# Performance work log

Measured on AMD Instinct MI355X. Metric: run time of the kernel, lower is better.

## Reference

```python
import jax, jax.numpy as jnp
import numpy as np

NUM_HEADS = 16


def rotate_half(x):
    # '... (j d) -> ... j d' with j=2: split last dim into two halves
    x1, x2 = jnp.split(x, 2, axis=-1)
    return jnp.concatenate([-x2, x1], axis=-1)


def apply_rotary_pos_emb(pos, t):
    # pos: [L, d] broadcast onto t: [B, H, L, d]
    return t * jnp.cos(pos) + rotate_half(t) * jnp.sin(pos)


def setup_inputs() -> dict:
    key = jax.random.key(0)
    ks = jax.random.split(key, 10)
    B, N, KV_N, C = 2, 2048, 2048, 1024
    hd = C // NUM_HEADS
    q = jax.random.normal(ks[0], (B, N, C), dtype=jnp.float32)
    k = jax.random.normal(ks[1], (B, KV_N, C), dtype=jnp.float32)
    v = jax.random.normal(ks[2], (B, KV_N, C), dtype=jnp.float32)
    mask = jax.random.randint(ks[3], (B, KV_N), 0, 2) > 0
    pos_emb = jax.random.normal(ks[4], (KV_N, hd), dtype=jnp.float32)
    s = 1.0 / np.sqrt(C)
    qW = jax.random.normal(ks[5], (C, C), dtype=jnp.float32) * s
    kW = jax.random.normal(ks[6], (C, C), dtype=jnp.float32) * s
    vW = jax.random.normal(ks[7], (C, C), dtype=jnp.float32) * s
    projW = jax.random.normal(ks[8], (C, C), dtype=jnp.float32) * s
    return {"q": q, "k": k, "v": v, "mask": mask, "pos_emb": pos_emb,
            "qW": qW, "kW": kW, "vW": vW, "projW": projW}


def reference(q, k, v, mask, pos_emb, qW, kW, vW, projW):
    B, N, C = q.shape
    H = NUM_HEADS
    hd = C // H
    scale = hd ** -0.5
    # linear projections (no bias)
    q = q @ qW
    k = k @ kW
    v = v @ vW
    # b l (h d) -> b h l d
    split = lambda t: t.reshape(t.shape[0], t.shape[1], H, hd).transpose(0, 2, 1, 3)
    q, k, v = split(q), split(k), split(v)
    q = q * scale
    # inline RoPE on q and k
    q = apply_rotary_pos_emb(pos_emb[:q.shape[-2]], q)
    k = apply_rotary_pos_emb(pos_emb[:k.shape[-2]], k)
    attn = jnp.einsum('bhid,bhjd->bhij', q, k)
    mask_value = -jnp.finfo(attn.dtype).max
    attn = jnp.where(mask[:, None, None, :], attn, mask_value)
    attn = jax.nn.softmax(attn, axis=-1)
    x = jnp.einsum('bhij,bhjd->bhid', attn, v)
    x = x.transpose(0, 2, 1, 3).reshape(B, N, C)
    return x @ projW
```

## Files before the change

kernel.cpp:

```cpp
#include <hip/hip_runtime.h>
#include <hip/hip_bf16.h>

#define BB 2
#define NN 2048
#define KVN 2048
#define CC 1024
#define HH 16
#define HD 64

typedef __bf16 bf16;
typedef __attribute__((ext_vector_type(4))) __bf16 bf16x4;
typedef __attribute__((ext_vector_type(8))) __bf16 bf16x8;
typedef __attribute__((ext_vector_type(4))) float f32x4;

__device__ __forceinline__ void gload_lds16(const void* g, void* l) {
  __builtin_amdgcn_global_load_lds(
      (const __attribute__((address_space(1))) void*)g,
      (__attribute__((address_space(3))) void*)l, 16, 0, 0);
}

__global__ __launch_bounds__(256)
void wtrans(const float* __restrict__ qW, const float* __restrict__ kW,
            const float* __restrict__ vW, const float* __restrict__ pW,
            bf16* __restrict__ Wt) {
  __shared__ bf16 t[64][72];
  const float* in = (blockIdx.z == 0) ? qW : (blockIdx.z == 1) ? kW
                    : (blockIdx.z == 2) ? vW : pW;
  bf16* out = Wt + (size_t)blockIdx.z * CC * CC;
  int r0 = blockIdx.y * 64, c0 = blockIdx.x * 64;
  int tid = threadIdx.x;
  int lr = tid >> 3, lc = (tid & 7) * 8;
  for (int p = 0; p < 2; ++p) {
    int rr = lr + p * 32;
    const float* src = &in[(size_t)(r0 + rr) * CC + c0 + lc];
    float4 a = *(const float4*)src;
    float4 b = *(const float4*)(src + 4);
    t[lc + 0][rr] = (bf16)a.x; t[lc + 1][rr] = (bf16)a.y;
    t[lc + 2][rr] = (bf16)a.z; t[lc + 3][rr] = (bf16)a.w;
    t[lc + 4][rr] = (bf16)b.x; t[lc + 5][rr] = (bf16)b.y;
    t[lc + 6][rr] = (bf16)b.z; t[lc + 7][rr] = (bf16)b.w;
  }
  __syncthreads();
  for (int p = 0; p < 2; ++p) {
    int rr = lr + p * 32;
    *(bf16x8*)&out[(size_t)(c0 + rr) * CC + r0 + lc] = *(const bf16x8*)&t[rr][lc];
  }
}

__global__ __launch_bounds__(256, 3)
void gemm_qkv(const float* __restrict__ qin, const float* __restrict__ kin,
              const float* __restrict__ vin, const bf16* __restrict__ Wt,
              const float* __restrict__ pos, bf16* __restrict__ Qp,
              bf16* __restrict__ Kp, bf16* __restrict__ Vp) {
  __shared__ bf16 As[128 * 64];
  __shared__ bf16 Bs[128 * 64];
  const int bid = blockIdx.x;
  const int u = bid & 7, s = bid >> 3;
  const int nblk = s >> 2;
  const int m0 = (u * 4 + (s & 3)) * 128;
  const int z = nblk >> 3;
  const int n0 = (nblk & 7) * 128;
  const float* A = (z == 0) ? qin : (z == 1) ? kin : vin;
  const bf16* Bt = Wt + (size_t)z * CC * CC;
  bf16* Out = (z == 0) ? Qp : (z == 1) ? Kp : Vp;
  const int tid = threadIdx.x;
  const int wave = tid >> 6, lane = tid & 63;
  const int quad = lane >> 4, l15 = lane & 15;
  const int waveM = (wave >> 1) * 64, waveN = (wave & 1) * 64;
  f32x4 acc[4][4] = {};

  for (int k0 = 0; k0 < CC; k0 += 64) {
#pragma unroll
    for (int p = 0; p < 4; ++p) {
      int ch = p * 256 + tid;
      int r = ch >> 3, c = (ch & 7) ^ (r & 7);
      gload_lds16(Bt + (size_t)(n0 + r) * CC + k0 + c * 8, &Bs[ch * 8]);
    }
#pragma unroll
    for (int p = 0; p < 4; ++p) {
      int ch = p * 256 + tid;
      int r = ch >> 3, c = (ch & 7) ^ (r & 7);
      const float* src = A + (size_t)(m0 + r) * CC + k0 + c * 8;
      float4 a0 = *(const float4*)src;
      float4 a1 = *(const float4*)(src + 4);
      bf16x8 t;
      t[0] = (bf16)a0.x; t[1] = (bf16)a0.y; t[2] = (bf16)a0.z; t[3] = (bf16)a0.w;
      t[4] = (bf16)a1.x; t[5] = (bf16)a1.y; t[6] = (bf16)a1.z; t[7] = (bf16)a1.w;
      *(bf16x8*)&As[ch * 8] = t;
    }
    __syncthreads();
    bf16x8 af[4][2], bfr[4][2];
#pragma unroll
    for (int i = 0; i < 4; ++i) {
      int rA = waveM + i * 16 + l15;
      af[i][0] = *(const bf16x8*)&As[(rA * 8 + (quad ^ (rA & 7))) * 8];
      af[i][1] = *(const bf16x8*)&As[(rA * 8 + ((quad + 4) ^ (rA & 7))) * 8];
      int rB = waveN + i * 16 + l15;
      bfr[i][0] = *(const bf16x8*)&Bs[(rB * 8 + (quad ^ (rB & 7))) * 8];
      bfr[i][1] = *(const bf16x8*)&Bs[(rB * 8 + ((quad + 4) ^ (rB & 7))) * 8];
    }
#pragma unroll
    for (int mi = 0; mi < 4; ++mi)
#pragma unroll
      for (int ni = 0; ni < 4; ++ni) {
        acc[mi][ni] = __builtin_amdgcn_mfma_f32_16x16x32_bf16(
            af[mi][0], bfr[ni][0], acc[mi][ni], 0, 0, 0);
        acc[mi][ni] = __builtin_amdgcn_mfma_f32_16x16x32_bf16(
            af[mi][1], bfr[ni][1], acc[mi][ni], 0, 0, 0);
      }
    __syncthreads();
  }
  const float scale = (z == 0) ? 0.125f : 1.0f;
#pragma unroll
  for (int mi = 0; mi < 4; ++mi) {
#pragma unroll
    for (int r = 0; r < 4; ++r) {
      int m = m0 + waveM + mi * 16 + quad * 4 + r;
      int l = m & (NN - 1);
      if (z == 2) {
#pragma unroll
        for (int ni = 0; ni < 4; ++ni)
          Out[(size_t)m * CC + n0 + waveN + ni * 16 + l15] = (bf16)acc[mi][ni][r];
      } else {
#pragma unroll
        for (int ni = 0; ni < 2; ++ni) {
          int col = n0 + waveN + ni * 16 + l15;
          int d = ni * 16 + l15;
          float x1 = acc[mi][ni][r], x2 = acc[mi][ni + 2][r];
          float s1, c1, s2f, c2f;
          __sincosf(pos[l * HD + d], &s1, &c1);
          __sincosf(pos[l * HD + d + 32], &s2f, &c2f);
          Out[(size_t)m * CC + col]      = (bf16)((x1 * c1 - x2 * s1) * scale);
          Out[(size_t)m * CC + col + 32] = (bf16)((x2 * c2f + x1 * s2f) * scale);
        }
      }
    }
  }
}

__global__ __launch_bounds__(256)
void kpack_kernel(const bf16* __restrict__ Kp, bf16* __restrict__ Kpack) {
  int tix = blockIdx.x, h = blockIdx.y, b = blockIdx.z;
  int bh = b * HH + h;
#pragma unroll
  for (int p = 0; p < 2; ++p) {
    int sp = p * 256 + threadIdx.x;
    int fs = sp >> 6, lane = sp & 63, quad = (sp >> 4) & 3, l15 = sp & 15;
    int ni = fs >> 1, hf = fs & 1;
    bf16x8 v = *(const bf16x8*)&Kp[((size_t)(b * KVN + tix * 64 + ni * 16 + l15)) * CC
                                   + h * HD + hf * 32 + quad * 8];
    *(bf16x8*)&Kpack[(((size_t)(bh * 32 + tix)) * 8 + fs) * 512 + lane * 8] = v;
  }
}

__global__ __launch_bounds__(256)
void vpack_kernel(const bf16* __restrict__ Vp, const int* __restrict__ mask,
                  bf16* __restrict__ VpA, bf16* __restrict__ VpB) {
  __shared__ bf16 t[64][80];
  int tix = blockIdx.x, h = blockIdx.y, b = blockIdx.z;
  int j0 = tix * 64, bh = b * HH + h;
  const int* maskb = mask + b * KVN;
  int tid = threadIdx.x;
  int lr = tid >> 3, lc = (tid & 7) * 8;
  for (int p = 0; p < 2; ++p) {
    int j = lr + p * 32;
    int mv = maskb[j0 + j];
    bf16x8 v = *(const bf16x8*)&Vp[(size_t)(b * KVN + j0 + j) * CC + h * HD + lc];
#pragma unroll
    for (int uu = 0; uu < 8; ++uu) t[lc + uu][j] = mv ? v[uu] : (bf16)0.f;
  }
  __syncthreads();
  for (int p = 0; p < 3; ++p) {
    int sp = p * 256 + tid;
    if (sp < 640) {
      int fs = sp >> 6, lane = sp & 63, quad = (sp >> 4) & 3, l15 = sp & 15;
      int ni = fs >> 1, hf = fs & 1;
      bf16x8 v;
      if (ni < 4) {
        v = *(const bf16x8*)&t[ni * 16 + l15][hf * 32 + quad * 8];
      } else {
#pragma unroll
        for (int jj = 0; jj < 8; ++jj)
          v[jj] = (l15 == 0) ? (bf16)(float)maskb[j0 + hf * 32 + quad * 8 + jj]
                             : (bf16)0.f;
      }
      bf16* dst = (fs < 6) ? (VpA + (size_t)fs * (1 << 19))
                           : (VpB + (size_t)(fs - 6) * (1 << 19));
      *(bf16x8*)&dst[((size_t)(bh * 32 + tix)) * 512 + lane * 8] = v;
    }
  }
}

__global__ __launch_bounds__(256, 2)
void attn3(const bf16* __restrict__ Qp, const bf16* __restrict__ Kpack,
           const bf16* __restrict__ VpA, const bf16* __restrict__ VpB,
           bf16* __restrict__ X) {
  __shared__ char smem[49152];
  const int tid = threadIdx.x, wave = tid >> 6, lane = tid & 63;
  const int quad = lane >> 4, l15 = lane & 15;
  const int bid = blockIdx.x;
  const int u = bid & 7, s = bid >> 3;
  const int bh = u * 4 + (s & 3), qp = s >> 2;
  const int b = bh >> 4, h = bh & 15;
  const int qc = qp * 2 + (wave >> 1), kh = wave & 1;
  const int q0 = qc * 64;
  const int sw = 2 * (l15 & 7);

  bf16* P = (bf16*)(smem + wave * 2048);
  float* mrg = (float*)(smem + 8192);

  bf16x8 qa[4][2];
#pragma unroll
  for (int g = 0; g < 4; ++g) {
    const bf16* qrow = Qp + ((size_t)(b * NN) + q0 + g * 16 + l15) * CC + h * HD;
    qa[g][0] = *(const bf16x8*)&qrow[quad * 8];
    qa[g][1] = *(const bf16x8*)&qrow[32 + quad * 8];
  }

  f32x4 Oacc[4][5] = {};
  const bf16* kbase = Kpack + (size_t)bh * 32 * 8 * 512;

  for (int it = 0; it < 16; ++it) {
    int t = kh * 16 + it;
    bf16x8 kb[8], vb[10];
#pragma unroll
    for (int fs = 0; fs < 8; ++fs)
      kb[fs] = *(const bf16x8*)&kbase[((size_t)t * 8 + fs) * 512 + lane * 8];
#pragma unroll
    for (int fs = 0; fs < 10; ++fs) {
      const bf16* vbs = (fs < 6) ? (VpA + (size_t)fs * (1 << 19))
                                 : (VpB + (size_t)(fs - 6) * (1 << 19));
      vb[fs] = *(const bf16x8*)&vbs[((size_t)(bh * 32 + t)) * 512 + lane * 8];
    }
#pragma unroll
    for (int g = 0; g < 4; ++g) {
      f32x4 sg[4];
#pragma unroll
      for (int ni = 0; ni < 4; ++ni) {
        f32x4 zz = {};
        zz = __builtin_amdgcn_mfma_f32_16x16x32_bf16(kb[ni * 2], qa[g][0], zz, 0, 0, 0);
        zz = __builtin_amdgcn_mfma_f32_16x16x32_bf16(kb[ni * 2 + 1], qa[g][1], zz, 0, 0, 0);
        sg[ni] = zz;
      }
#pragma unroll
      for (int ni = 0; ni < 4; ++ni) {
        bf16x4 pk;
#pragma unroll
        for (int r = 0; r < 4; ++r) pk[r] = (bf16)__expf(sg[ni][r] - 4.0f);
        *(bf16x4*)&P[(l15 * 16 + ((ni * 4 + quad) ^ sw)) * 4] = pk;
      }
      bf16x8 pf0 = *(const bf16x8*)&P[(l15 * 16 + ((quad * 2) ^ sw)) * 4];
      bf16x8 pf1 = *(const bf16x8*)&P[(l15 * 16 + ((8 + quad * 2) ^ sw)) * 4];
#pragma unroll
      for (int ni = 0; ni < 5; ++ni) {
        Oacc[g][ni] = __builtin_amdgcn_mfma_f32_16x16x32_bf16(vb[ni * 2], pf0, Oacc[g][ni], 0, 0, 0);
        Oacc[g][ni] = __builtin_amdgcn_mfma_f32_16x16x32_bf16(vb[ni * 2 + 1], pf1, Oacc[g][ni], 0, 0, 0);
      }
    }
  }
  if (kh == 1) {
    float* dst = mrg + (wave >> 1) * 5120 + lane * 4;
#pragma unroll
    for (int g = 0; g < 4; ++g)
#pragma unroll
      for (int ni = 0; ni < 5; ++ni)
        *(f32x4*)&dst[(g * 5 + ni) * 256] = Oacc[g][ni];
  }
  __syncthreads();
  if (kh == 0) {
    float* src = mrg + (wave >> 1) * 5120 + lane * 4;
#pragma unroll
    for (int g = 0; g < 4; ++g) {
#pragma unroll
      for (int ni = 0; ni < 5; ++ni) {
        f32x4 o = *(const f32x4*)&src[(g * 5 + ni) * 256];
#pragma unroll
        for (int r = 0; r < 4; ++r) Oacc[g][ni][r] += o[r];
      }
      float ls = __shfl(Oacc[g][4][0], l15, 64);
      float rn = 1.0f / ls;
#pragma unroll
      for (int ni = 0; ni < 4; ++ni) {
        bf16x4 ov;
#pragma unroll
        for (int r = 0; r < 4; ++r) ov[r] = (bf16)(Oacc[g][ni][r] * rn);
        *(bf16x4*)&X[((size_t)(b * NN) + q0 + g * 16 + l15) * CC
                     + h * HD + ni * 16 + quad * 4] = ov;
      }
    }
  }
}

__global__ __launch_bounds__(256, 4)
void gemm_proj(const bf16* __restrict__ A, const bf16* __restrict__ Bt,
               float* __restrict__ Out) {
  __shared__ bf16 As[64 * 64];
  __shared__ bf16 Bs[128 * 64];
  const int bid = blockIdx.x;
  const int u = bid & 7, s = bid >> 3;
  const int m0 = (u * 8 + (s >> 3)) * 64;
  const int n0 = (s & 7) * 128;
  const int tid = threadIdx.x;
  const int wave = tid >> 6, lane = tid & 63;
  const int quad = lane >> 4, l15 = lane & 15;
  const int waveM = (wave >> 1) * 32, waveN = (wave & 1) * 64;
  f32x4 acc[2][4] = {};

  for (int k0 = 0; k0 < CC; k0 += 64) {
#pragma unroll
    for (int p = 0; p < 2; ++p) {
      int ch = p * 256 + tid;
      int r = ch >> 3, c = (ch & 7) ^ (r & 7);
      gload_lds16(A + (size_t)(m0 + r) * CC + k0 + c * 8, &As[ch * 8]);
    }
#pragma unroll
    for (int p = 0; p < 4; ++p) {
      int ch = p * 256 + tid;
      int r = ch >> 3, c = (ch & 7) ^ (r & 7);
      gload_lds16(Bt + (size_t)(n0 + r) * CC + k0 + c * 8, &Bs[ch * 8]);
    }
    __syncthreads();
    bf16x8 af[2][2], bfr[4][2];
#pragma unroll
    for (int i = 0; i < 2; ++i) {
      int rA = waveM + i * 16 + l15;
      af[i][0] = *(const bf16x8*)&As[(rA * 8 + (quad ^ (rA & 7))) * 8];
      af[i][1] = *(const bf16x8*)&As[(rA * 8 + ((quad + 4) ^ (rA & 7))) * 8];
    }
#pragma unroll
    for (int i = 0; i < 4; ++i) {
      int rB = waveN + i * 16 + l15;
      bfr[i][0] = *(const bf16x8*)&Bs[(rB * 8 + (quad ^ (rB & 7))) * 8];
      bfr[i][1] = *(const bf16x8*)&Bs[(rB * 8 + ((quad + 4) ^ (rB & 7))) * 8];
    }
#pragma unroll
    for (int mi = 0; mi < 2; ++mi)
#pragma unroll
      for (int ni = 0; ni < 4; ++ni) {
        acc[mi][ni] = __builtin_amdgcn_mfma_f32_16x16x32_bf16(
            af[mi][0], bfr[ni][0], acc[mi][ni], 0, 0, 0);
        acc[mi][ni] = __builtin_amdgcn_mfma_f32_16x16x32_bf16(
            af[mi][1], bfr[ni][1], acc[mi][ni], 0, 0, 0);
      }
    __syncthreads();
  }
#pragma unroll
  for (int mi = 0; mi < 2; ++mi)
#pragma unroll
    for (int ni = 0; ni < 4; ++ni)
#pragma unroll
      for (int r = 0; r < 4; ++r) {
        int row = m0 + waveM + mi * 16 + quad * 4 + r;
        int col = n0 + waveN + ni * 16 + l15;
        Out[(size_t)row * CC + col] = acc[mi][ni][r];
      }
}

extern "C" void kernel_launch(void* const* d_in, const int* in_sizes, int n_in,
                              void* d_out, int out_size, void* d_ws, size_t ws_size,
                              hipStream_t stream) {
  const float* q    = (const float*)d_in[0];
  const float* k    = (const float*)d_in[1];
  const float* v    = (const float*)d_in[2];
  const int*   mask = (const int*)d_in[3];
  const float* pos  = (const float*)d_in[4];
  const float* qW   = (const float*)d_in[5];
  const float* kW   = (const float*)d_in[6];
  const float* vW   = (const float*)d_in[7];
  const float* pW   = (const float*)d_in[8];
  float* out = (float*)d_out;

  char* w = (char*)d_ws;
  const size_t MB = 1024 * 1024;
  bf16* Wt    = (bf16*)(w);
  bf16* Qp    = (bf16*)(w + 8 * MB);
  bf16* Kp    = (bf16*)(w + 16 * MB);
  bf16* Vp    = (bf16*)(w + 24 * MB);
  bf16* Kpack = (bf16*)(w + 32 * MB);
  bf16* VpA   = (bf16*)(w);
  bf16* VpB   = (bf16*)(w + 40 * MB);
  bf16* X     = (bf16*)(w + 16 * MB);

  wtrans<<<dim3(16, 16, 4), 256, 0, stream>>>(qW, kW, vW, pW, Wt);
  gemm_qkv<<<dim3(768), 256, 0, stream>>>(q, k, v, Wt, pos, Qp, Kp, Vp);
  kpack_kernel<<<dim3(KVN / 64, HH, BB), 256, 0, stream>>>(Kp, Kpack);
  vpack_kernel<<<dim3(KVN / 64, HH, BB), 256, 0, stream>>>(Vp, mask, VpA, VpB);
  attn3<<<dim3(512), 256, 0, stream>>>(Qp, Kpack, VpA, VpB, X);
  gemm_proj<<<dim3(512), 256, 0, stream>>>(X, Wt + 3 * (size_t)CC * CC, out);
}
```

Measured before the change: 224.7 us.

## Stream K/V tiles through double-buffered LDS and drop the K packing kernel

Removes the separate kpack kernel. The attention kernel now loads K tiles straight from the projected K buffer into swizzled LDS with global_load_lds, and V fragments likewise, using double buffering so the next tile's load overlaps current compute. Blocks shrink to 128 threads, and each wave covers the full KV range for its 64 query rows, so the cross-wave LDS merge of partial outputs goes away. The trade-off is fewer waves per block, a block barrier every tile, and LDS bank-conflict behaviour that now depends on the swizzle.

```diff
diff --git a/kernel.cpp b/kernel.cpp
--- a/kernel.cpp
+++ b/kernel.cpp
@@ -139,21 +139,6 @@
 }
 
 __global__ __launch_bounds__(256)
-void kpack_kernel(const bf16* __restrict__ Kp, bf16* __restrict__ Kpack) {
-  int tix = blockIdx.x, h = blockIdx.y, b = blockIdx.z;
-  int bh = b * HH + h;
-#pragma unroll
-  for (int p = 0; p < 2; ++p) {
-    int sp = p * 256 + threadIdx.x;
-    int fs = sp >> 6, lane = sp & 63, quad = (sp >> 4) & 3, l15 = sp & 15;
-    int ni = fs >> 1, hf = fs & 1;
-    bf16x8 v = *(const bf16x8*)&Kp[((size_t)(b * KVN + tix * 64 + ni * 16 + l15)) * CC
-                                   + h * HD + hf * 32 + quad * 8];
-    *(bf16x8*)&Kpack[(((size_t)(bh * 32 + tix)) * 8 + fs) * 512 + lane * 8] = v;
-  }
-}
-
-__global__ __launch_bounds__(256)
 void vpack_kernel(const bf16* __restrict__ Vp, const int* __restrict__ mask,
                   bf16* __restrict__ VpA, bf16* __restrict__ VpB) {
   __shared__ bf16 t[64][80];
@@ -191,23 +176,22 @@
   }
 }
 
-__global__ __launch_bounds__(256, 2)
-void attn3(const bf16* __restrict__ Qp, const bf16* __restrict__ Kpack,
+__global__ __launch_bounds__(128, 2)
+void attn4(const bf16* __restrict__ Qp, const bf16* __restrict__ Kp,
            const bf16* __restrict__ VpA, const bf16* __restrict__ VpB,
            bf16* __restrict__ X) {
-  __shared__ char smem[49152];
+  __shared__ bf16 Ks[2][64 * 64];
+  __shared__ bf16 Vs[2][640 * 8];
+  __shared__ bf16 Ps[2][1024];
   const int tid = threadIdx.x, wave = tid >> 6, lane = tid & 63;
   const int quad = lane >> 4, l15 = lane & 15;
   const int bid = blockIdx.x;
   const int u = bid & 7, s = bid >> 3;
   const int bh = u * 4 + (s & 3), qp = s >> 2;
   const int b = bh >> 4, h = bh & 15;
-  const int qc = qp * 2 + (wave >> 1), kh = wave & 1;
-  const int q0 = qc * 64;
+  const int q0 = qp * 128 + wave * 64;
   const int sw = 2 * (l15 & 7);
-
-  bf16* P = (bf16*)(smem + wave * 2048);
-  float* mrg = (float*)(smem + 8192);
+  bf16* P = Ps[wave];
 
   bf16x8 qa[4][2];
 #pragma unroll
@@ -218,28 +202,51 @@
   }
 
   f32x4 Oacc[4][5] = {};
-  const bf16* kbase = Kpack + (size_t)bh * 32 * 8 * 512;
-
-  for (int it = 0; it < 16; ++it) {
-    int t = kh * 16 + it;
-    bf16x8 kb[8], vb[10];
-#pragma unroll
-    for (int fs = 0; fs < 8; ++fs)
-      kb[fs] = *(const bf16x8*)&kbase[((size_t)t * 8 + fs) * 512 + lane * 8];
-#pragma unroll
-    for (int fs = 0; fs < 10; ++fs) {
-      const bf16* vbs = (fs < 6) ? (VpA + (size_t)fs * (1 << 19))
-                                 : (VpB + (size_t)(fs - 6) * (1 << 19));
-      vb[fs] = *(const bf16x8*)&vbs[((size_t)(bh * 32 + t)) * 512 + lane * 8];
-    }
+
+#define STAGE(t, bufi)                                                        \
+  {                                                                           \
+    _Pragma("unroll") for (int p = 0; p < 9; ++p) {                           \
+      int ch = p * 128 + tid;                                                 \
+      if (ch < 512) {                                                         \
+        int r = ch >> 3, c = (ch & 7) ^ (r & 7);                              \
+        gload_lds16(Kp + ((size_t)(b * KVN + (t) * 64 + r)) * CC + h * HD + c * 8, \
+                    &Ks[bufi][ch * 8]);                                       \
+      } else {                                                                \
+        int idx = ch - 512;                                                   \
+        int fs = idx >> 6, ln = idx & 63;                                     \
+        const bf16* vbs = (fs < 6) ? (VpA + (size_t)fs * (1 << 19))           \
+                                   : (VpB + (size_t)(fs - 6) * (1 << 19));    \
+        gload_lds16(vbs + ((size_t)(bh * 32 + (t))) * 512 + ln * 8,           \
+                    &Vs[bufi][idx * 8]);                                      \
+      }                                                                       \
+    }                                                                         \
+  }
+
+  STAGE(0, 0);
+  __syncthreads();
+
+  for (int t = 0; t < 32; ++t) {
+    const int buf = t & 1;
+    bf16x8 kb[4][2], vb[10];
+#pragma unroll
+    for (int ni = 0; ni < 4; ++ni) {
+      int rk = ni * 16 + l15;
+#pragma unroll
+      for (int hf = 0; hf < 2; ++hf)
+        kb[ni][hf] = *(const bf16x8*)&Ks[buf][(rk * 8 + ((hf * 4 + quad) ^ (rk & 7))) * 8];
+    }
+#pragma unroll
+    for (int fs = 0; fs < 10; ++fs)
+      vb[fs] = *(const bf16x8*)&Vs[buf][(fs * 64 + lane) * 8];
+    if (t + 1 < 32) STAGE(t + 1, buf ^ 1);
 #pragma unroll
     for (int g = 0; g < 4; ++g) {
       f32x4 sg[4];
 #pragma unroll
       for (int ni = 0; ni < 4; ++ni) {
         f32x4 zz = {};
-        zz = __builtin_amdgcn_mfma_f32_16x16x32_bf16(kb[ni * 2], qa[g][0], zz, 0, 0, 0);
-        zz = __builtin_amdgcn_mfma_f32_16x16x32_bf16(kb[ni * 2 + 1], qa[g][1], zz, 0, 0, 0);
+        zz = __builtin_amdgcn_mfma_f32_16x16x32_bf16(kb[ni][0], qa[g][0], zz, 0, 0, 0);
+        zz = __builtin_amdgcn_mfma_f32_16x16x32_bf16(kb[ni][1], qa[g][1], zz, 0, 0, 0);
         sg[ni] = zz;
       }
 #pragma unroll
@@ -257,36 +264,20 @@
         Oacc[g][ni] = __builtin_amdgcn_mfma_f32_16x16x32_bf16(vb[ni * 2 + 1], pf1, Oacc[g][ni], 0, 0, 0);
       }
     }
-  }
-  if (kh == 1) {
-    float* dst = mrg + (wave >> 1) * 5120 + lane * 4;
-#pragma unroll
-    for (int g = 0; g < 4; ++g)
-#pragma unroll
-      for (int ni = 0; ni < 5; ++ni)
-        *(f32x4*)&dst[(g * 5 + ni) * 256] = Oacc[g][ni];
-  }
-  __syncthreads();
-  if (kh == 0) {
-    float* src = mrg + (wave >> 1) * 5120 + lane * 4;
-#pragma unroll
-    for (int g = 0; g < 4; ++g) {
-#pragma unroll
-      for (int ni = 0; ni < 5; ++ni) {
-        f32x4 o = *(const f32x4*)&src[(g * 5 + ni) * 256];
-#pragma unroll
-        for (int r = 0; r < 4; ++r) Oacc[g][ni][r] += o[r];
-      }
-      float ls = __shfl(Oacc[g][4][0], l15, 64);
-      float rn = 1.0f / ls;
-#pragma unroll
-      for (int ni = 0; ni < 4; ++ni) {
-        bf16x4 ov;
-#pragma unroll
-        for (int r = 0; r < 4; ++r) ov[r] = (bf16)(Oacc[g][ni][r] * rn);
-        *(bf16x4*)&X[((size_t)(b * NN) + q0 + g * 16 + l15) * CC
-                     + h * HD + ni * 16 + quad * 4] = ov;
-      }
+    __syncthreads();
+  }
+#undef STAGE
+#pragma unroll
+  for (int g = 0; g < 4; ++g) {
+    float ls = __shfl(Oacc[g][4][0], l15, 64);
+    float rn = 1.0f / ls;
+#pragma unroll
+    for (int ni = 0; ni < 4; ++ni) {
+      bf16x4 ov;
+#pragma unroll
+      for (int r = 0; r < 4; ++r) ov[r] = (bf16)(Oacc[g][ni][r] * rn);
+      *(bf16x4*)&X[((size_t)(b * NN) + q0 + g * 16 + l15) * CC
+                   + h * HD + ni * 16 + quad * 4] = ov;
     }
   }
 }
@@ -372,19 +363,17 @@
 
   char* w = (char*)d_ws;
   const size_t MB = 1024 * 1024;
-  bf16* Wt    = (bf16*)(w);
-  bf16* Qp    = (bf16*)(w + 8 * MB);
-  bf16* Kp    = (bf16*)(w + 16 * MB);
-  bf16* Vp    = (bf16*)(w + 24 * MB);
-  bf16* Kpack = (bf16*)(w + 32 * MB);
-  bf16* VpA   = (bf16*)(w);
-  bf16* VpB   = (bf16*)(w + 40 * MB);
-  bf16* X     = (bf16*)(w + 16 * MB);
+  bf16* Wt  = (bf16*)(w);
+  bf16* Qp  = (bf16*)(w + 8 * MB);
+  bf16* Kp  = (bf16*)(w + 16 * MB);
+  bf16* Vp  = (bf16*)(w + 24 * MB);
+  bf16* VpA = (bf16*)(w);
+  bf16* VpB = (bf16*)(w + 32 * MB);
+  bf16* X   = (bf16*)(w + 36 * MB);
 
   wtrans<<<dim3(16, 16, 4), 256, 0, stream>>>(qW, kW, vW, pW, Wt);
   gemm_qkv<<<dim3(768), 256, 0, stream>>>(q, k, v, Wt, pos, Qp, Kp, Vp);
-  kpack_kernel<<<dim3(KVN / 64, HH, BB), 256, 0, stream>>>(Kp, Kpack);
   vpack_kernel<<<dim3(KVN / 64, HH, BB), 256, 0, stream>>>(Vp, mask, VpA, VpB);
-  attn3<<<dim3(512), 256, 0, stream>>>(Qp, Kpack, VpA, VpB, X);
+  attn4<<<dim3(512), 128, 0, stream>>>(Qp, Kp, VpA, VpB, X);
   gemm_proj<<<dim3(512), 256, 0, stream>>>(X, Wt + 3 * (size_t)CC * CC, out);
 }
```

Measured after the change: 252.1 us. +12.2%, slower.
